# Kernel tuning notes

Hardware: AMD Instinct MI355X
Metric: run time of the kernel (lower is better)

The kernel has to match this reference:

```python
import jax, jax.numpy as jnp
import numpy as np

BITS = 16          # number of histogram bins == number of spiking time steps
B, IN_DIM, HID = 16384, 784, 128


def setup_inputs() -> dict:
    key = jax.random.key(0)
    ks = jax.random.split(key, 9)
    dims = [(HID, IN_DIM), (HID, HID), (HID, HID), (IN_DIM, HID)]
    inp = {"features": jax.random.uniform(ks[0], (B, IN_DIM), jnp.float32)}
    for i, (o, d) in enumerate(dims):
        inp["W%d" % i] = jax.random.normal(ks[1 + i], (o, d), jnp.float32) * 0.05
        inp["b%d" % i] = jax.random.normal(ks[5 + i], (o,), jnp.float32) * 0.05
    # np.histogram_bin_edges(bins=16) -> 17 uniformly spaced edges per layer
    in_max = [1.0, 4.0, 4.0, 4.0]
    out_max = [4.0, 4.0, 4.0, 4.0]
    for i in range(4):
        inp["in_bins%d" % i] = jnp.linspace(0.0, in_max[i], BITS + 1, dtype=jnp.float32)
        inp["out_bins%d" % i] = jnp.linspace(0.0, out_max[i], BITS + 1, dtype=jnp.float32)
    return inp


def _spike(t):
    # output[output>1]=1; output[output<1]=0  (==1 stays 1)  -> (t >= 1)
    # totals[output==1] -= 1
    s = (t >= 1.0).astype(t.dtype)
    return s, t - s


def _forward(features, Ws, bs, in_bins, out_bins):
    h_in = [e[1] - e[0] for e in in_bins]    # uniform spike heights
    h_out = [e[1] - e[0] for e in out_bins]
    # set_up_weights: weight *= h_in; weight /= h_out (bias likewise)
    Weff = [Ws[l] * (h_in[l] / h_out[l]) for l in range(4)]
    beff = [bs[l] * (h_in[l] / h_out[l]) for l in range(4)]
    n = features.shape[0]
    # discretize: np.digitize(x, in_bins) - 1, then / 16.0 (non-differentiable)
    act = (jnp.digitize(jax.lax.stop_gradient(features), in_bins[0]) - 1).astype(features.dtype) / BITS
    t_in = jnp.zeros_like(features)                               # input-layer membrane
    totals = tuple(jnp.broadcast_to(beff[l], (n,) + beff[l].shape) for l in range(4))  # reset_totals: totals = bias
    out_acc = jnp.zeros((n, Weff[3].shape[0]), features.dtype)

    def step(carry, _):
        t_in, t0, t1, t2, t3, out = carry
        s_in, t_in = _spike(t_in + act)
        # process_layer: totals += sum(weight * spikes, axis=1) == spikes @ W.T
        s0, t0 = _spike(t0 + s_in @ Weff[0].T)
        s1, t1 = _spike(t1 + s0 @ Weff[1].T)
        s2, t2 = _spike(t2 + s1 @ Weff[2].T)
        s3, t3 = _spike(t3 + s2 @ Weff[3].T)
        return (t_in, t0, t1, t2, t3, out + s3), None

    carry, _ = jax.lax.scan(step, (t_in,) + totals + (out_acc,), None, length=BITS)
    out_spikes = carry[-1]
    # decoder_output_layer.reconstruct: spikes * (out_bins[1] - out_bins[0])
    return out_spikes * h_out[3]


def reference(features, W0, W1, W2, W3, b0, b1, b2, b3,
              in_bins0, in_bins1, in_bins2, in_bins3,
              out_bins0, out_bins1, out_bins2, out_bins3):
    return _forward(features,
                    [W0, W1, W2, W3], [b0, b1, b2, b3],
                    [in_bins0, in_bins1, in_bins2, in_bins3],
                    [out_bins0, out_bins1, out_bins2, out_bins3])
```

## Files before the change

### kernel.cpp

```cpp
#include <hip/hip_runtime.h>

#define IN_DIM 784
#define HID 128
#define NSTEP 16
#define BATCH 16384

constexpr int W0T_OFF = 0;
constexpr int W1T_OFF = W0T_OFF + IN_DIM*HID;
constexpr int W2T_OFF = W1T_OFF + HID*HID;
constexpr int W3T_OFF = W2T_OFF + HID*HID;
constexpr int B0_OFF  = W3T_OFF + HID*IN_DIM;
constexpr int B1_OFF  = B0_OFF + HID;
constexpr int B2_OFF  = B1_OFF + HID;
constexpr int B3_OFF  = B2_OFF + HID;
constexpr int WS_FLOATS = B3_OFF + IN_DIM;

constexpr int CHUNK_COLS = 32;
constexpr int CHUNK_F    = CHUNK_COLS * HID;
constexpr int NCHUNK     = 25;

__global__ __launch_bounds__(256) void prep_kernel(
    const float* __restrict__ W0, const float* __restrict__ b0,
    const float* __restrict__ W1, const float* __restrict__ b1,
    const float* __restrict__ W2, const float* __restrict__ b2,
    const float* __restrict__ W3, const float* __restrict__ b3,
    const float* __restrict__ ib0, const float* __restrict__ ob0,
    const float* __restrict__ ib1, const float* __restrict__ ob1,
    const float* __restrict__ ib2, const float* __restrict__ ob2,
    const float* __restrict__ ib3, const float* __restrict__ ob3,
    float* __restrict__ ws)
{
    int idx = blockIdx.x * 256 + threadIdx.x;
    if (idx >= WS_FLOATS) return;
    float r0 = (ib0[1] - ib0[0]) / (ob0[1] - ob0[0]);
    float r1 = (ib1[1] - ib1[0]) / (ob1[1] - ob1[0]);
    float r2 = (ib2[1] - ib2[0]) / (ob2[1] - ob2[0]);
    float r3 = (ib3[1] - ib3[0]) / (ob3[1] - ob3[0]);
    if (idx < W1T_OFF) {
        int t = idx;            int k = t >> 7, j = t & 127;
        ws[idx] = W0[j * IN_DIM + k] * r0;
    } else if (idx < W2T_OFF) {
        int t = idx - W1T_OFF;  int k = t >> 7, j = t & 127;
        ws[idx] = W1[j * HID + k] * r1;
    } else if (idx < W3T_OFF) {
        int t = idx - W2T_OFF;  int k = t >> 7, j = t & 127;
        ws[idx] = W2[j * HID + k] * r2;
    } else if (idx < B0_OFF) {
        int t = idx - W3T_OFF;  int k = t / IN_DIM, o = t % IN_DIM;
        ws[idx] = W3[o * HID + k] * r3;
    } else if (idx < B1_OFF) ws[idx] = b0[idx - B0_OFF] * r0;
    else if (idx < B2_OFF)   ws[idx] = b1[idx - B1_OFF] * r1;
    else if (idx < B3_OFF)   ws[idx] = b2[idx - B2_OFF] * r2;
    else                     ws[idx] = b3[idx - B3_OFF] * r3;
}

__global__ __launch_bounds__(256) void snn_main(
    const float* __restrict__ feat,
    const float* __restrict__ ws,
    const float* __restrict__ ib0,
    const float* __restrict__ ob3,
    float* __restrict__ out)
{
    __shared__ float smem[2 * CHUNK_F];

    const int tid  = threadIdx.x;
    const int lane = tid & 63;
    const int wid  = tid >> 6;
    const int sample = blockIdx.x * 4 + wid;

    const float* W0t = ws + W0T_OFF;
    const float* W1t = ws + W1T_OFF;
    const float* W2t = ws + W2T_OFF;
    const float* W3t = ws + W3T_OFF;
    const float* frow = feat + (size_t)sample * IN_DIM;

    float edge[16];
#pragma unroll
    for (int e = 0; e < 16; ++e) edge[e] = ib0[e + 1];

    {
        const float4* g4 = (const float4*)W0t;
        float4* lb = (float4*)smem;
#pragma unroll
        for (int i = 0; i < 4; ++i) lb[i * 256 + tid] = g4[i * 256 + tid];
    }
    __syncthreads();

    float2 C[16];
#pragma unroll
    for (int mv = 0; mv < 16; ++mv) C[mv] = make_float2(0.f, 0.f);

    for (int c = 0; c < NCHUNK; ++c) {
        float4 rg0, rg1, rg2, rg3;
        {
            const float4* g4 = (const float4*)W0t + (size_t)(c + 1) * (CHUNK_F / 4);
            rg0 = g4[0 * 256 + tid];
            rg1 = g4[1 * 256 + tid];
            rg2 = g4[2 * 256 + tid];
            rg3 = g4[3 * 256 + tid];
        }

        int col = c * CHUNK_COLS + (lane & 31);
        bool valid = col < IN_DIM;
        float x = frow[valid ? col : 0];
        int mm = 0;
#pragma unroll
        for (int e = 0; e < 16; ++e) mm += (x >= edge[e]) ? 1 : 0;
        if (!valid) mm = -1;

        const float2* bufp = (const float2*)(smem + (c & 1) * CHUNK_F);
#pragma unroll
        for (int mv = 1; mv <= 16; ++mv) {
            unsigned mk = (unsigned)__ballot(mm == mv);
            float2 ca = make_float2(0.f, 0.f), cb = make_float2(0.f, 0.f);
            while (mk) {
                int b0 = __builtin_ctz(mk); mk &= mk - 1;
                float2 w0 = bufp[b0 * 64 + lane];
                if (mk) {
                    int b1 = __builtin_ctz(mk); mk &= mk - 1;
                    float2 w1 = bufp[b1 * 64 + lane];
                    if (mk) {
                        int b2 = __builtin_ctz(mk); mk &= mk - 1;
                        float2 w2 = bufp[b2 * 64 + lane];
                        if (mk) {
                            int b3i = __builtin_ctz(mk); mk &= mk - 1;
                            float2 w3 = bufp[b3i * 64 + lane];
                            cb.x += w3.x; cb.y += w3.y;
                        }
                        ca.x += w2.x; ca.y += w2.y;
                    }
                    cb.x += w1.x; cb.y += w1.y;
                }
                ca.x += w0.x; ca.y += w0.y;
            }
            C[mv - 1].x += ca.x + cb.x;
            C[mv - 1].y += ca.y + cb.y;
        }

        if (c + 1 < NCHUNK) {
            float4* lb = (float4*)(smem + ((c + 1) & 1) * CHUNK_F);
            lb[0 * 256 + tid] = rg0;
            lb[1 * 256 + tid] = rg1;
            lb[2 * 256 + tid] = rg2;
            lb[3 * 256 + tid] = rg3;
        }
        __syncthreads();
    }

    float2 t0 = ((const float2*)(ws + B0_OFF))[lane];
    float2 t1 = ((const float2*)(ws + B1_OFF))[lane];
    float2 t2 = ((const float2*)(ws + B2_OFF))[lane];
    float4 t3[4], cnt[4];
    {
        const float4* b3v = (const float4*)(ws + B3_OFF);
#pragma unroll
        for (int r = 0; r < 3; ++r) t3[r] = b3v[r * 64 + lane];
        t3[3] = make_float4(0.f, 0.f, 0.f, 0.f);
        if (lane < 4) t3[3] = b3v[192 + lane];
#pragma unroll
        for (int r = 0; r < 4; ++r) cnt[r] = make_float4(0.f, 0.f, 0.f, 0.f);
    }

    for (int s = 1; s <= NSTEP; ++s) {
#pragma unroll
        for (int mv = 1; mv <= 16; ++mv) {
            if (((s * mv) & 15) < mv) { t0.x += C[mv - 1].x; t0.y += C[mv - 1].y; }
        }
        {
            bool px = (t0.x >= 1.0f), py = (t0.y >= 1.0f);
            unsigned long long mx = __ballot(px);
            unsigned long long my = __ballot(py);
            if (px) t0.x -= 1.0f;
            if (py) t0.y -= 1.0f;
            float2 ca = make_float2(0.f, 0.f), cb = make_float2(0.f, 0.f);
            while (mx) {
                int b0 = __builtin_ctzll(mx); mx &= mx - 1;
                float2 w0 = ((const float2*)(W1t + (2 * b0) * HID))[lane];
                if (mx) {
                    int b1 = __builtin_ctzll(mx); mx &= mx - 1;
                    float2 w1 = ((const float2*)(W1t + (2 * b1) * HID))[lane];
                    if (mx) {
                        int b2 = __builtin_ctzll(mx); mx &= mx - 1;
                        float2 w2 = ((const float2*)(W1t + (2 * b2) * HID))[lane];
                        if (mx) {
                            int b3i = __builtin_ctzll(mx); mx &= mx - 1;
                            float2 w3 = ((const float2*)(W1t + (2 * b3i) * HID))[lane];
                            cb.x += w3.x; cb.y += w3.y;
                        }
                        ca.x += w2.x; ca.y += w2.y;
                    }
                    cb.x += w1.x; cb.y += w1.y;
                }
                ca.x += w0.x; ca.y += w0.y;
            }
            while (my) {
                int b0 = __builtin_ctzll(my); my &= my - 1;
                float2 w0 = ((const float2*)(W1t + (2 * b0 + 1) * HID))[lane];
                if (my) {
                    int b1 = __builtin_ctzll(my); my &= my - 1;
                    float2 w1 = ((const float2*)(W1t + (2 * b1 + 1) * HID))[lane];
                    if (my) {
                        int b2 = __builtin_ctzll(my); my &= my - 1;
                        float2 w2 = ((const float2*)(W1t + (2 * b2 + 1) * HID))[lane];
                        if (my) {
                            int b3i = __builtin_ctzll(my); my &= my - 1;
                            float2 w3 = ((const float2*)(W1t + (2 * b3i + 1) * HID))[lane];
                            cb.x += w3.x; cb.y += w3.y;
                        }
                        ca.x += w2.x; ca.y += w2.y;
                    }
                    cb.x += w1.x; cb.y += w1.y;
                }
                ca.x += w0.x; ca.y += w0.y;
            }
            t1.x += ca.x + cb.x; t1.y += ca.y + cb.y;
        }
        {
            bool px = (t1.x >= 1.0f), py = (t1.y >= 1.0f);
            unsigned long long mx = __ballot(px);
            unsigned long long my = __ballot(py);
            if (px) t1.x -= 1.0f;
            if (py) t1.y -= 1.0f;
            float2 ca = make_float2(0.f, 0.f), cb = make_float2(0.f, 0.f);
            while (mx) {
                int b0 = __builtin_ctzll(mx); mx &= mx - 1;
                float2 w0 = ((const float2*)(W2t + (2 * b0) * HID))[lane];
                if (mx) {
                    int b1 = __builtin_ctzll(mx); mx &= mx - 1;
                    float2 w1 = ((const float2*)(W2t + (2 * b1) * HID))[lane];
                    if (mx) {
                        int b2 = __builtin_ctzll(mx); mx &= mx - 1;
                        float2 w2 = ((const float2*)(W2t + (2 * b2) * HID))[lane];
                        if (mx) {
                            int b3i = __builtin_ctzll(mx); mx &= mx - 1;
                            float2 w3 = ((const float2*)(W2t + (2 * b3i) * HID))[lane];
                            cb.x += w3.x; cb.y += w3.y;
                        }
                        ca.x += w2.x; ca.y += w2.y;
                    }
                    cb.x += w1.x; cb.y += w1.y;
                }
                ca.x += w0.x; ca.y += w0.y;
            }
            while (my) {
                int b0 = __builtin_ctzll(my); my &= my - 1;
                float2 w0 = ((const float2*)(W2t + (2 * b0 + 1) * HID))[lane];
                if (my) {
                    int b1 = __builtin_ctzll(my); my &= my - 1;
                    float2 w1 = ((const float2*)(W2t + (2 * b1 + 1) * HID))[lane];
                    if (my) {
                        int b2 = __builtin_ctzll(my); my &= my - 1;
                        float2 w2 = ((const float2*)(W2t + (2 * b2 + 1) * HID))[lane];
                        if (my) {
                            int b3i = __builtin_ctzll(my); my &= my - 1;
                            float2 w3 = ((const float2*)(W2t + (2 * b3i + 1) * HID))[lane];
                            cb.x += w3.x; cb.y += w3.y;
                        }
                        ca.x += w2.x; ca.y += w2.y;
                    }
                    cb.x += w1.x; cb.y += w1.y;
                }
                ca.x += w0.x; ca.y += w0.y;
            }
            t2.x += ca.x + cb.x; t2.y += ca.y + cb.y;
        }
        {
            bool px = (t2.x >= 1.0f), py = (t2.y >= 1.0f);
            unsigned long long mx = __ballot(px);
            unsigned long long my = __ballot(py);
            if (px) t2.x -= 1.0f;
            if (py) t2.y -= 1.0f;
            while (mx) {
                int b0 = __builtin_ctzll(mx); mx &= mx - 1;
                const float4* c0 = (const float4*)(W3t + (2 * b0) * IN_DIM);
                float4 x0 = c0[lane], x1 = c0[64 + lane], x2 = c0[128 + lane];
                float4 x3 = c0[192 + (lane & 3)];
                if (mx) {
                    int b1 = __builtin_ctzll(mx); mx &= mx - 1;
                    const float4* c1 = (const float4*)(W3t + (2 * b1) * IN_DIM);
                    float4 y0 = c1[lane], y1 = c1[64 + lane], y2 = c1[128 + lane];
                    float4 y3 = c1[192 + (lane & 3)];
                    t3[0].x += y0.x; t3[0].y += y0.y; t3[0].z += y0.z; t3[0].w += y0.w;
                    t3[1].x += y1.x; t3[1].y += y1.y; t3[1].z += y1.z; t3[1].w += y1.w;
                    t3[2].x += y2.x; t3[2].y += y2.y; t3[2].z += y2.z; t3[2].w += y2.w;
                    if (lane < 4) { t3[3].x += y3.x; t3[3].y += y3.y; t3[3].z += y3.z; t3[3].w += y3.w; }
                }
                t3[0].x += x0.x; t3[0].y += x0.y; t3[0].z += x0.z; t3[0].w += x0.w;
                t3[1].x += x1.x; t3[1].y += x1.y; t3[1].z += x1.z; t3[1].w += x1.w;
                t3[2].x += x2.x; t3[2].y += x2.y; t3[2].z += x2.z; t3[2].w += x2.w;
                if (lane < 4) { t3[3].x += x3.x; t3[3].y += x3.y; t3[3].z += x3.z; t3[3].w += x3.w; }
            }
            while (my) {
                int b0 = __builtin_ctzll(my); my &= my - 1;
                const float4* c0 = (const float4*)(W3t + (2 * b0 + 1) * IN_DIM);
                float4 x0 = c0[lane], x1 = c0[64 + lane], x2 = c0[128 + lane];
                float4 x3 = c0[192 + (lane & 3)];
                if (my) {
                    int b1 = __builtin_ctzll(my); my &= my - 1;
                    const float4* c1 = (const float4*)(W3t + (2 * b1 + 1) * IN_DIM);
                    float4 y0 = c1[lane], y1 = c1[64 + lane], y2 = c1[128 + lane];
                    float4 y3 = c1[192 + (lane & 3)];
                    t3[0].x += y0.x; t3[0].y += y0.y; t3[0].z += y0.z; t3[0].w += y0.w;
                    t3[1].x += y1.x; t3[1].y += y1.y; t3[1].z += y1.z; t3[1].w += y1.w;
                    t3[2].x += y2.x; t3[2].y += y2.y; t3[2].z += y2.z; t3[2].w += y2.w;
                    if (lane < 4) { t3[3].x += y3.x; t3[3].y += y3.y; t3[3].z += y3.z; t3[3].w += y3.w; }
                }
                t3[0].x += x0.x; t3[0].y += x0.y; t3[0].z += x0.z; t3[0].w += x0.w;
                t3[1].x += x1.x; t3[1].y += x1.y; t3[1].z += x1.z; t3[1].w += x1.w;
                t3[2].x += x2.x; t3[2].y += x2.y; t3[2].z += x2.z; t3[2].w += x2.w;
                if (lane < 4) { t3[3].x += x3.x; t3[3].y += x3.y; t3[3].z += x3.z; t3[3].w += x3.w; }
            }
        }
#pragma unroll
        for (int r = 0; r < 4; ++r) {
            if (t3[r].x >= 1.0f) { t3[r].x -= 1.0f; cnt[r].x += 1.0f; }
            if (t3[r].y >= 1.0f) { t3[r].y -= 1.0f; cnt[r].y += 1.0f; }
            if (t3[r].z >= 1.0f) { t3[r].z -= 1.0f; cnt[r].z += 1.0f; }
            if (t3[r].w >= 1.0f) { t3[r].w -= 1.0f; cnt[r].w += 1.0f; }
        }
    }

    const float h = ob3[1] - ob3[0];
    float4* orow = (float4*)(out + (size_t)sample * IN_DIM);
#pragma unroll
    for (int r = 0; r < 3; ++r)
        orow[r * 64 + lane] = make_float4(cnt[r].x * h, cnt[r].y * h, cnt[r].z * h, cnt[r].w * h);
    if (lane < 4)
        orow[192 + lane] = make_float4(cnt[3].x * h, cnt[3].y * h, cnt[3].z * h, cnt[3].w * h);
}

extern "C" void kernel_launch(void* const* d_in, const int* in_sizes, int n_in,
                              void* d_out, int out_size, void* d_ws, size_t ws_size,
                              hipStream_t stream)
{
    const float* feat = (const float*)d_in[0];
    const float* W0  = (const float*)d_in[1];
    const float* b0  = (const float*)d_in[2];
    const float* W1  = (const float*)d_in[3];
    const float* b1  = (const float*)d_in[4];
    const float* W2  = (const float*)d_in[5];
    const float* b2  = (const float*)d_in[6];
    const float* W3  = (const float*)d_in[7];
    const float* b3  = (const float*)d_in[8];
    const float* ib0 = (const float*)d_in[9];
    const float* ob0 = (const float*)d_in[10];
    const float* ib1 = (const float*)d_in[11];
    const float* ob1 = (const float*)d_in[12];
    const float* ib2 = (const float*)d_in[13];
    const float* ob2 = (const float*)d_in[14];
    const float* ib3 = (const float*)d_in[15];
    const float* ob3 = (const float*)d_in[16];
    float* ws  = (float*)d_ws;
    float* op  = (float*)d_out;

    prep_kernel<<<(WS_FLOATS + 255) / 256, 256, 0, stream>>>(
        W0, b0, W1, b1, W2, b2, W3, b3,
        ib0, ob0, ib1, ob1, ib2, ob2, ib3, ob3, ws);

    snn_main<<<BATCH / 4, 256, 0, stream>>>(feat, ws, ib0, ob3, op);
}
```

Baseline: 409.4 us.

## Use 512-thread blocks with single-buffered W0 chunk in shared memory

Doubles the block size to 8 waves (8 samples per block), so each staged W0 chunk is shared by twice as many samples and each thread loads half as much. Drops the double-buffered shared memory to a single 16KB buffer with an extra barrier before overwriting, which lowers LDS use per block and raises the launch-bounds occupancy hint. The cost is an added __syncthreads per chunk and possible register pressure from the tighter occupancy target. The hidden part of the kernel, which still assumes waves per block via wid, must stay consistent.

```diff
diff --git a/kernel.cpp b/kernel.cpp
--- a/kernel.cpp
+++ b/kernel.cpp
@@ -18,6 +18,9 @@
 constexpr int CHUNK_COLS = 32;
 constexpr int CHUNK_F    = CHUNK_COLS * HID;
 constexpr int NCHUNK     = 25;
+
+constexpr int TPB   = 512;
+constexpr int WAVES = TPB / 64;
 
 __global__ __launch_bounds__(256) void prep_kernel(
     const float* __restrict__ W0, const float* __restrict__ b0,
@@ -54,19 +57,19 @@
     else                     ws[idx] = b3[idx - B3_OFF] * r3;
 }
 
-__global__ __launch_bounds__(256) void snn_main(
+__global__ __launch_bounds__(TPB, 8) void snn_main(
     const float* __restrict__ feat,
     const float* __restrict__ ws,
     const float* __restrict__ ib0,
     const float* __restrict__ ob3,
     float* __restrict__ out)
 {
-    __shared__ float smem[2 * CHUNK_F];
+    __shared__ float smem[CHUNK_F];
 
     const int tid  = threadIdx.x;
     const int lane = tid & 63;
     const int wid  = tid >> 6;
-    const int sample = blockIdx.x * 4 + wid;
+    const int sample = blockIdx.x * WAVES + wid;
 
     const float* W0t = ws + W0T_OFF;
     const float* W1t = ws + W1T_OFF;
@@ -82,7 +85,7 @@
         const float4* g4 = (const float4*)W0t;
         float4* lb = (float4*)smem;
 #pragma unroll
-        for (int i = 0; i < 4; ++i) lb[i * 256 + tid] = g4[i * 256 + tid];
+        for (int i = 0; i < 2; ++i) lb[i * TPB + tid] = g4[i * TPB + tid];
     }
     __syncthreads();
 
@@ -91,13 +94,11 @@
     for (int mv = 0; mv < 16; ++mv) C[mv] = make_float2(0.f, 0.f);
 
     for (int c = 0; c < NCHUNK; ++c) {
-        float4 rg0, rg1, rg2, rg3;
+        float4 rg0, rg1;
         {
             const float4* g4 = (const float4*)W0t + (size_t)(c + 1) * (CHUNK_F / 4);
-            rg0 = g4[0 * 256 + tid];
-            rg1 = g4[1 * 256 + tid];
-            rg2 = g4[2 * 256 + tid];
-            rg3 = g4[3 * 256 + tid];
+            rg0 = g4[0 * TPB + tid];
+            rg1 = g4[1 * TPB + tid];
         }
 
         int col = c * CHUNK_COLS + (lane & 31);
@@ -108,7 +109,7 @@
         for (int e = 0; e < 16; ++e) mm += (x >= edge[e]) ? 1 : 0;
         if (!valid) mm = -1;
 
-        const float2* bufp = (const float2*)(smem + (c & 1) * CHUNK_F);
+        const float2* bufp = (const float2*)smem;
 #pragma unroll
         for (int mv = 1; mv <= 16; ++mv) {
             unsigned mk = (unsigned)__ballot(mm == mv);
@@ -137,14 +138,13 @@
             C[mv - 1].y += ca.y + cb.y;
         }
 
+        __syncthreads();
         if (c + 1 < NCHUNK) {
-            float4* lb = (float4*)(smem + ((c + 1) & 1) * CHUNK_F);
-            lb[0 * 256 + tid] = rg0;
-            lb[1 * 256 + tid] = rg1;
-            lb[2 * 256 + tid] = rg2;
-            lb[3 * 256 + tid] = rg3;
-        }
-        __syncthreads();
+            float4* lb = (float4*)smem;
+            lb[0 * TPB + tid] = rg0;
+            lb[1 * TPB + tid] = rg1;
+            __syncthreads();
+        }
     }
 
     float2 t0 = ((const float2*)(ws + B0_OFF))[lane];
@@ -357,5 +357,5 @@
         W0, b0, W1, b1, W2, b2, W3, b3,
         ib0, ob0, ib1, ob1, ib2, ob2, ib3, ob3, ws);
 
-    snn_main<<<BATCH / 4, 256, 0, stream>>>(feat, ws, ib0, ob3, op);
+    snn_main<<<BATCH / WAVES, TPB, 0, stream>>>(feat, ws, ib0, ob3, op);
 }
```

Result: slower. 1.564 ms (+282.1%).
